# Kernel optimization log

Hardware: AMD Instinct MI355X
Metric: run time of the kernel (lower is better)

The kernel has to match this reference:

```python
import math
import jax, jax.numpy as jnp
import numpy as np

B, T, D = 16, 512, 64  # N = B*T = 8192


def setup_inputs() -> dict:
    key = jax.random.key(0)
    k1, k2, k3, k4 = jax.random.split(key, 4)
    z_seq = jax.random.normal(k1, (B, T, D), dtype=jnp.float32)
    prior_mean = jax.random.normal(k2, (D,), dtype=jnp.float32) * 0.1
    prior_std = jax.random.uniform(k3, (D,), dtype=jnp.float32, minval=0.5, maxval=1.5)
    z_prior = jax.random.normal(k4, (B * T, D), dtype=jnp.float32)
    return {"z_seq": z_seq, "prior_mean": prior_mean, "prior_std": prior_std, "z_prior": z_prior}


def _sq_dists(x, y):
    # squared euclidean distances, [n, m]; clamp tiny negatives from cancellation
    xx = jnp.sum(x * x, axis=-1)
    yy = jnp.sum(y * y, axis=-1)
    d2 = xx[:, None] + yy[None, :] - 2.0 * (x @ y.T)
    return jnp.maximum(d2, 0.0)


def _rbf(x, y, sigma):
    return jnp.exp(-_sq_dists(x, y) / (2.0 * sigma * sigma))


def reference(z_seq, prior_mean, prior_std, z_prior):
    d = z_seq.shape[-1]
    sigma = math.sqrt(d)
    z = z_seq.reshape(-1, d)                      # [N, d]
    z_norm = (z - prior_mean) / prior_std          # [N, d]
    x, y = z_norm, z_prior
    n, m = x.shape[0], y.shape[0]
    kxx = _rbf(x, x, sigma)
    kyy = _rbf(y, y, sigma)
    kxy = _rbf(x, y, sigma)
    mmd = ((kxx.sum() - jnp.trace(kxx)) / (n * (n - 1))
           + (kyy.sum() - jnp.trace(kyy)) / (m * (m - 1))
           - 2.0 * kxy.mean())
    return jnp.maximum(mmd, 0.0)
```

## Files before the change

### kernel.cpp

```cpp
#include <hip/hip_runtime.h>
#include <hip/hip_bf16.h>
#include <math.h>


using short8  = __attribute__((ext_vector_type(8))) short;
using f32x4   = __attribute__((ext_vector_type(4))) float;
using float4v = __attribute__((ext_vector_type(4))) float;

#define NROWS 8192
#define DDIM  64
#define GRID_MAIN (4096 + 2 * 2080)

#define PRESCALE 0.15014030109830622f

__device__ __forceinline__ float exp2_fast(float x) {
#if __has_builtin(__builtin_amdgcn_exp2f)
    return __builtin_amdgcn_exp2f(x);
#else
    return exp2f(x);
#endif
}

__global__ __launch_bounds__(256) void mmd_prep(
    const float* __restrict__ z_seq, const float* __restrict__ pmean,
    const float* __restrict__ pstd, const float* __restrict__ z_prior,
    __hip_bfloat16* __restrict__ Xb, __hip_bfloat16* __restrict__ Yb,
    float* __restrict__ sxx, float* __restrict__ syy)
{
    const int tid  = threadIdx.x;
    const int lane = tid & 63;
    const int wid  = tid >> 6;
    const int w    = blockIdx.x * 4 + wid;
    const int sub  = lane >> 4;
    const int row  = w * 4 + sub;
    const int d0   = (lane & 15) * 4;

    float4v v;
    __hip_bfloat16* dst;
    float* sdst;
    int r;
    if (row < NROWS) {
        r = row;
        float4v z  = *reinterpret_cast<const float4v*>(z_seq + (size_t)r * DDIM + d0);
        float4v pm = *reinterpret_cast<const float4v*>(pmean + d0);
        float4v ps = *reinterpret_cast<const float4v*>(pstd + d0);
#pragma unroll
        for (int k = 0; k < 4; ++k) v[k] = (z[k] - pm[k]) / ps[k];
        dst = Xb; sdst = sxx;
    } else {
        r = row - NROWS;
        v = *reinterpret_cast<const float4v*>(z_prior + (size_t)r * DDIM + d0);
        dst = Yb; sdst = syy;
    }

    ushort4 hb;
    float sq = 0.0f;
#pragma unroll
    for (int k = 0; k < 4; ++k) {
        __hip_bfloat16 b = __float2bfloat16(v[k] * PRESCALE);
        reinterpret_cast<__hip_bfloat16*>(&hb)[k] = b;
        float vb = __bfloat162float(b);
        sq += vb * vb;
    }
    *reinterpret_cast<ushort4*>(dst + (size_t)r * DDIM + d0) = hb;

#pragma unroll
    for (int off = 8; off; off >>= 1) sq += __shfl_xor(sq, off, 64);
    if ((lane & 15) == 0) sdst[r] = 0.5f * sq;
}

__global__ __launch_bounds__(256) void mmd_main(
    const __hip_bfloat16* __restrict__ Xb, const __hip_bfloat16* __restrict__ Yb,
    const float* __restrict__ sxx, const float* __restrict__ syy,
    double* __restrict__ partials)
{
    __shared__ __align__(16) char Bs[16384];

    const int bid = blockIdx.x;

    int bi, bj;
    bool sym;
    const __hip_bfloat16* A;
    const __hip_bfloat16* Bp;
    const float* sa;
    const float* sb;

    if (bid < 4096) {
        sym = false;
        bi = bid >> 6; bj = bid & 63;
        A = Xb; Bp = Yb; sa = sxx; sb = syy;
    } else {
        sym = true;
        const int t = bid - 4096;
        const int u = t >> 1;
        int b = (int)((sqrtf((float)(8 * u + 1)) - 1.0f) * 0.5f);
        while ((b + 1) * (b + 2) / 2 <= u) ++b;
        while (b * (b + 1) / 2 > u) --b;
        bj = b;
        bi = u - b * (b + 1) / 2;
        if (t & 1) { A = Yb; Bp = Yb; sa = syy; sb = syy; }
        else       { A = Xb; Bp = Xb; sa = sxx; sb = sxx; }
    }

    const int tid  = threadIdx.x;
    const int lane = tid & 63;
    const int wid  = tid >> 6;
    const int quad = lane >> 4;
    const int l15  = lane & 15;

    const int iBlock = bi * 128;
    const int jBlock = bj * 128;

    {
        const char* gB = (const char*)Bp + (size_t)jBlock * 128;
#pragma unroll
        for (int k = 0; k < 4; ++k) {
            const int c  = wid * 4 + k;
            const int x  = c * 1024 + lane * 16;
            const int gx = x ^ (((x >> 7) & 7) << 4);
            __builtin_amdgcn_global_load_lds(
                (const __attribute__((address_space(1))) void*)(gB + gx),
                (__attribute__((address_space(3))) void*)(Bs + c * 1024),
                16, 0, 0);
        }
    }

    const int i0 = iBlock + wid * 32;

    short8 af[2][2];
    f32x4  nsx[2];
#pragma unroll
    for (int mt = 0; mt < 2; ++mt) {
        const int ar = i0 + mt * 16 + l15;
#pragma unroll
        for (int ks = 0; ks < 2; ++ks)
            af[mt][ks] = *reinterpret_cast<const short8*>(
                A + (size_t)ar * DDIM + ks * 32 + quad * 8);
        f32x4 s4 = *reinterpret_cast<const f32x4*>(sa + i0 + mt * 16 + quad * 4);
        nsx[mt] = -s4;
    }

    float nsy[8];
#pragma unroll
    for (int nt = 0; nt < 8; ++nt) nsy[nt] = -sb[jBlock + l15 + nt * 16];

    __syncthreads();

    const int swz   = (l15 & 7) << 4;
    const int off0  = (quad * 16) ^ swz;
    const int off1  = (quad * 16 + 64) ^ swz;
    const char* lb0 = Bs + l15 * 128;

    float ls0 = 0.0f, ls1 = 0.0f, ls2 = 0.0f, ls3 = 0.0f;

#pragma unroll
    for (int nt = 0; nt < 8; ++nt) {
        const int jt = jBlock + nt * 16;
        if (sym && jt < i0) continue;

        const char* lp = lb0 + nt * 16 * 128;
        short8 b0 = *reinterpret_cast<const short8*>(lp + off0);
        short8 b1 = *reinterpret_cast<const short8*>(lp + off1);

#pragma unroll
        for (int mt = 0; mt < 2; ++mt) {
            const int it = i0 + mt * 16;
            if (sym && jt < it) continue;

            f32x4 acc4;
#pragma unroll
            for (int r = 0; r < 4; ++r) acc4[r] = nsx[mt][r] + nsy[nt];
            acc4 = __builtin_amdgcn_mfma_f32_16x16x32_bf16(af[mt][0], b0, acc4, 0, 0, 0);
            acc4 = __builtin_amdgcn_mfma_f32_16x16x32_bf16(af[mt][1], b1, acc4, 0, 0, 0);

            if (sym && jt == it) {
                ls0 += (l15 > quad * 4 + 0) ? exp2_fast(acc4[0]) : 0.0f;
                ls1 += (l15 > quad * 4 + 1) ? exp2_fast(acc4[1]) : 0.0f;
                ls2 += (l15 > quad * 4 + 2) ? exp2_fast(acc4[2]) : 0.0f;
                ls3 += (l15 > quad * 4 + 3) ? exp2_fast(acc4[3]) : 0.0f;
            } else {
                ls0 += exp2_fast(acc4[0]);
                ls1 += exp2_fast(acc4[1]);
                ls2 += exp2_fast(acc4[2]);
                ls3 += exp2_fast(acc4[3]);
            }
        }
    }

    float lsum = (ls0 + ls1) + (ls2 + ls3);

#pragma unroll
    for (int off = 32; off; off >>= 1) lsum += __shfl_xor(lsum, off, 64);

    __shared__ float ws4[4];
    if (lane == 0) ws4[wid] = lsum;
    __syncthreads();
    if (tid == 0) {
        double tot = (double)ws4[0] + (double)ws4[1] + (double)ws4[2] + (double)ws4[3];
        partials[bid] = tot;
    }
}

__global__ __launch_bounds__(256) void mmd_final(
    const double* __restrict__ partials, float* __restrict__ out)
{
    const int tid = threadIdx.x;
    const double cs = 2.0 / (8192.0 * 8191.0);
    const double cx = -2.0 / (8192.0 * 8192.0);

    double s = 0.0;
    for (int idx = tid; idx < GRID_MAIN; idx += 256) {
        double c = (idx < 4096) ? cx : cs;
        s += partials[idx] * c;
    }
#pragma unroll
    for (int off = 32; off; off >>= 1) s += __shfl_xor(s, off, 64);

    __shared__ double wsum[4];
    const int lane = tid & 63, wid = tid >> 6;
    if (lane == 0) wsum[wid] = s;
    __syncthreads();
    if (tid == 0) {
        double mmd = wsum[0] + wsum[1] + wsum[2] + wsum[3];
        out[0] = (float)(mmd > 0.0 ? mmd : 0.0);
    }
}

extern "C" void kernel_launch(void* const* d_in, const int* in_sizes, int n_in,
                              void* d_out, int out_size, void* d_ws, size_t ws_size,
                              hipStream_t stream) {
    const float* z_seq   = (const float*)d_in[0];
    const float* pmean   = (const float*)d_in[1];
    const float* pstd    = (const float*)d_in[2];
    const float* z_prior = (const float*)d_in[3];
    float* out = (float*)d_out;

    char* ws = (char*)d_ws;
    __hip_bfloat16* Xb = (__hip_bfloat16*)(ws);
    __hip_bfloat16* Yb = (__hip_bfloat16*)(ws + (1u << 20));
    float* sxx = (float*)(ws + (2u << 20));
    float* syy = (float*)(ws + (2u << 20) + 32768);
    double* partials = (double*)(ws + (2u << 20) + 65536);

    mmd_prep<<<dim3(1024), dim3(256), 0, stream>>>(
        z_seq, pmean, pstd, z_prior, Xb, Yb, sxx, syy);
    mmd_main<<<dim3(GRID_MAIN), dim3(256), 0, stream>>>(
        Xb, Yb, sxx, syy, partials);
    mmd_final<<<dim3(1), dim3(256), 0, stream>>>(partials, out);
}
```

Measured before the change: 104.4 us.

## Enlarge row tile to 512 per block, reusing the LDS column tile across chunks

Each block now covers 512 rows against one 128-column tile, looping over four 128-row chunks while keeping the B tile resident in LDS. This cuts the main grid from 8256 to 2112 blocks. The symmetric-tile index mapping is reworked to enumerate the new triangular 512x128 block layout. The aim is less redundant B-tile loading and less per-block setup. In exchange, A fragments for each chunk are loaded serially without prefetch, and fewer blocks leave less parallelism to hide that latency. Symmetric blocks near the diagonal exit early, which can unbalance the load.

```diff
diff --git a/kernel.cpp b/kernel.cpp
--- a/kernel.cpp
+++ b/kernel.cpp
@@ -9,7 +9,7 @@
 
 #define NROWS 8192
 #define DDIM  64
-#define GRID_MAIN (4096 + 2 * 2080)
+#define GRID_MAIN (1024 + 2 * 544)
 
 #define PRESCALE 0.15014030109830622f
 
@@ -85,19 +85,21 @@
     const float* sa;
     const float* sb;
 
-    if (bid < 4096) {
+    if (bid < 1024) {
         sym = false;
         bi = bid >> 6; bj = bid & 63;
         A = Xb; Bp = Yb; sa = sxx; sb = syy;
     } else {
         sym = true;
-        const int t = bid - 4096;
+        const int t = bid - 1024;
         const int u = t >> 1;
-        int b = (int)((sqrtf((float)(8 * u + 1)) - 1.0f) * 0.5f);
-        while ((b + 1) * (b + 2) / 2 <= u) ++b;
-        while (b * (b + 1) / 2 > u) --b;
-        bj = b;
-        bi = u - b * (b + 1) / 2;
+        int g = (int)((sqrtf((float)(2 * u + 1)) - 1.0f) * 0.5f);
+        while (2 * (g + 1) * (g + 2) <= u) ++g;
+        while (2 * g * (g + 1) > u) --g;
+        const int rem = u - 2 * g * (g + 1);
+        const int q   = rem / (g + 1);
+        bj = 4 * g + q;
+        bi = rem - q * (g + 1);
         if (t & 1) { A = Yb; Bp = Yb; sa = syy; sb = syy; }
         else       { A = Xb; Bp = Xb; sa = sxx; sb = sxx; }
     }
@@ -108,7 +110,7 @@
     const int quad = lane >> 4;
     const int l15  = lane & 15;
 
-    const int iBlock = bi * 128;
+    const int iBlock = bi * 512;
     const int jBlock = bj * 128;
 
     {
@@ -125,7 +127,7 @@
         }
     }
 
-    const int i0 = iBlock + wid * 32;
+    int i0 = iBlock + wid * 32;
 
     short8 af[2][2];
     f32x4  nsx[2];
@@ -153,37 +155,55 @@
 
     float ls0 = 0.0f, ls1 = 0.0f, ls2 = 0.0f, ls3 = 0.0f;
 
-#pragma unroll
-    for (int nt = 0; nt < 8; ++nt) {
-        const int jt = jBlock + nt * 16;
-        if (sym && jt < i0) continue;
-
-        const char* lp = lb0 + nt * 16 * 128;
-        short8 b0 = *reinterpret_cast<const short8*>(lp + off0);
-        short8 b1 = *reinterpret_cast<const short8*>(lp + off1);
-
-#pragma unroll
-        for (int mt = 0; mt < 2; ++mt) {
-            const int it = i0 + mt * 16;
-            if (sym && jt < it) continue;
-
-            f32x4 acc4;
-#pragma unroll
-            for (int r = 0; r < 4; ++r) acc4[r] = nsx[mt][r] + nsy[nt];
-            acc4 = __builtin_amdgcn_mfma_f32_16x16x32_bf16(af[mt][0], b0, acc4, 0, 0, 0);
-            acc4 = __builtin_amdgcn_mfma_f32_16x16x32_bf16(af[mt][1], b1, acc4, 0, 0, 0);
-
-            if (sym && jt == it) {
-                ls0 += (l15 > quad * 4 + 0) ? exp2_fast(acc4[0]) : 0.0f;
-                ls1 += (l15 > quad * 4 + 1) ? exp2_fast(acc4[1]) : 0.0f;
-                ls2 += (l15 > quad * 4 + 2) ? exp2_fast(acc4[2]) : 0.0f;
-                ls3 += (l15 > quad * 4 + 3) ? exp2_fast(acc4[3]) : 0.0f;
-            } else {
-                ls0 += exp2_fast(acc4[0]);
-                ls1 += exp2_fast(acc4[1]);
-                ls2 += exp2_fast(acc4[2]);
-                ls3 += exp2_fast(acc4[3]);
+    for (int c = 0; c < 4; ++c) {
+#pragma unroll
+        for (int nt = 0; nt < 8; ++nt) {
+            const int jt = jBlock + nt * 16;
+            if (sym && jt < i0) continue;
+
+            const char* lp = lb0 + nt * 16 * 128;
+            short8 b0 = *reinterpret_cast<const short8*>(lp + off0);
+            short8 b1 = *reinterpret_cast<const short8*>(lp + off1);
+
+#pragma unroll
+            for (int mt = 0; mt < 2; ++mt) {
+                const int it = i0 + mt * 16;
+                if (sym && jt < it) continue;
+
+                f32x4 acc4;
+#pragma unroll
+                for (int r = 0; r < 4; ++r) acc4[r] = nsx[mt][r] + nsy[nt];
+                acc4 = __builtin_amdgcn_mfma_f32_16x16x32_bf16(af[mt][0], b0, acc4, 0, 0, 0);
+                acc4 = __builtin_amdgcn_mfma_f32_16x16x32_bf16(af[mt][1], b1, acc4, 0, 0, 0);
+
+                if (sym && jt == it) {
+                    ls0 += (l15 > quad * 4 + 0) ? exp2_fast(acc4[0]) : 0.0f;
+                    ls1 += (l15 > quad * 4 + 1) ? exp2_fast(acc4[1]) : 0.0f;
+                    ls2 += (l15 > quad * 4 + 2) ? exp2_fast(acc4[2]) : 0.0f;
+                    ls3 += (l15 > quad * 4 + 3) ? exp2_fast(acc4[3]) : 0.0f;
+                } else {
+                    ls0 += exp2_fast(acc4[0]);
+                    ls1 += exp2_fast(acc4[1]);
+                    ls2 += exp2_fast(acc4[2]);
+                    ls3 += exp2_fast(acc4[3]);
+                }
             }
+        }
+
+        if (c < 3) {
+            const int i0n = i0 + 128;
+            if (sym && jBlock + 112 < i0n) break;
+#pragma unroll
+            for (int mt = 0; mt < 2; ++mt) {
+                const int ar = i0n + mt * 16 + l15;
+#pragma unroll
+                for (int ks = 0; ks < 2; ++ks)
+                    af[mt][ks] = *reinterpret_cast<const short8*>(
+                        A + (size_t)ar * DDIM + ks * 32 + quad * 8);
+                f32x4 s4 = *reinterpret_cast<const f32x4*>(sa + i0n + mt * 16 + quad * 4);
+                nsx[mt] = -s4;
+            }
+            i0 = i0n;
         }
     }
 
@@ -210,7 +230,7 @@
 
     double s = 0.0;
     for (int idx = tid; idx < GRID_MAIN; idx += 256) {
-        double c = (idx < 4096) ? cx : cs;
+        double c = (idx < 1024) ? cx : cs;
         s += partials[idx] * c;
     }
 #pragma unroll
```

Result: faster. 100.8 us (-3.5%).
